# Performance work log

Measured on AMD Instinct MI355X. Metric: run time of the kernel, lower is better.

## Reference

```python
import jax, jax.numpy as jnp
import numpy as np

B, T, D, H = 64, 512, 512, 128

def swish(x):
    return x * jax.nn.sigmoid(x)

def setup_inputs() -> dict:
    key = jax.random.key(0)
    ks = jax.random.split(key, 8)
    X = jax.random.normal(ks[0], (B, T, D), dtype=jnp.float32)
    # strictly-upper-triangular random binary adjacency -> valid DAG
    adj = jax.random.bernoulli(ks[1], 0.3, (T, T)).astype(jnp.float32)
    dag = jnp.triu(adj, k=1)
    s = 1.0 / np.sqrt(D)
    Wk = jax.random.normal(ks[2], (H, D), dtype=jnp.float32) * s
    bk = jax.random.normal(ks[3], (H,), dtype=jnp.float32) * 0.01
    Wq = jax.random.normal(ks[4], (H, D), dtype=jnp.float32) * s
    bq = jax.random.normal(ks[5], (H,), dtype=jnp.float32) * 0.01
    Wv = jax.random.normal(ks[6], (H, D), dtype=jnp.float32) * s
    bv = jax.random.normal(ks[7], (H,), dtype=jnp.float32) * 0.01
    return {"X": X, "dag": dag, "Wk": Wk, "bk": bk, "Wq": Wq, "bq": bq, "Wv": Wv, "bv": bv}

def reference(X, dag, Wk, bk, Wq, bq, Wv, bv):
    K = swish(jnp.einsum('btd,hd->bth', X, Wk) + bk)  # [B,T,H]
    Q = swish(jnp.einsum('btd,hd->bth', X, Wq) + bq)
    V = swish(jnp.einsum('btd,hd->bth', X, Wv) + bv)
    S_qk = jnp.einsum('bqh,bkh->bqk', Q, K) / jnp.sqrt(jnp.float32(H))  # [B,T,T]
    dagT = dag.T  # [T,T]
    Sprime = dagT * jnp.einsum('ij,bjk->bik', dagT, S_qk)  # [B,T,T]
    # masked_fill(Sprime == 0, -inf) then softmax; rows that are all -inf
    # would produce NaN in torch and are replaced by zeros -> do it nan-free.
    nz = Sprime != 0
    masked = jnp.where(nz, Sprime, -jnp.inf)
    row_valid = jnp.any(nz, axis=-1, keepdims=True)  # [B,T,1]
    masked_safe = jnp.where(row_valid, masked, 0.0)
    probs = jax.nn.softmax(masked_safe, axis=-1) * row_valid  # [B,T,T]
    Vprime = jnp.einsum('ij,bjh->bih', dagT, V)  # [B,T,H]
    O = jnp.einsum('bqk,bkh->bqh', probs, V) + Vprime
    return O
```

## Files before the change

kernel.cpp:

```cpp
#include <hip/hip_runtime.h>
#include <hip/hip_bf16.h>

#define Bn 64
#define Tn 512
#define Dn 512
#define Hn 128
#define BT (Bn*Tn)

typedef unsigned short u16;
typedef unsigned long long u64;
typedef __attribute__((ext_vector_type(8))) short bf16x8;
typedef __attribute__((ext_vector_type(4))) float f32x4;

__device__ __forceinline__ u16 f2bf(float f) {
  union { float f; unsigned u; } v; v.f = f;
  unsigned r = (v.u + 0x7FFFu + ((v.u >> 16) & 1u)) >> 16;
  return (u16)r;
}

__device__ __forceinline__ bf16x8 pack8(float4 a, float4 b) {
  bf16x8 o;
  o[0] = (short)f2bf(a.x); o[1] = (short)f2bf(a.y);
  o[2] = (short)f2bf(a.z); o[3] = (short)f2bf(a.w);
  o[4] = (short)f2bf(b.x); o[5] = (short)f2bf(b.y);
  o[6] = (short)f2bf(b.z); o[7] = (short)f2bf(b.w);
  return o;
}

__device__ __forceinline__ void gload16(const void* g, void* lds) {
  __builtin_amdgcn_global_load_lds(
      (const __attribute__((address_space(1))) unsigned int*)g,
      (__attribute__((address_space(3))) unsigned int*)lds, 16, 0, 0);
}

__global__ __launch_bounds__(256) void prep(
    const float4* __restrict__ Wk, const float4* __restrict__ Wq,
    const float4* __restrict__ Wv, ushort4* __restrict__ Wcat,
    const float* __restrict__ dag, u16* __restrict__ dagT,
    u64* __restrict__ bits) {
  __shared__ float s[64][65];
  if (blockIdx.x < 192) {
    int idx = blockIdx.x * 256 + threadIdx.x;
    int which = idx >> 14, j = idx & 16383;
    const float4* src = (which == 0) ? Wk : (which == 1) ? Wq : Wv;
    float4 v = src[j];
    ushort4 o; o.x = f2bf(v.x); o.y = f2bf(v.y); o.z = f2bf(v.z); o.w = f2bf(v.w);
    Wcat[idx] = o;
  } else {
    int bid = blockIdx.x - 192;
    int bx = bid & 7, by = bid >> 3;
    int r0 = by * 64, c0 = bx * 64;
    int t = threadIdx.x;
    int c4 = t & 15, rr = t >> 4;
#pragma unroll
    for (int q = 0; q < 4; ++q) {
      int r = rr + q * 16;
      float4 v = *(const float4*)&dag[(size_t)(r0 + r) * Tn + c0 + c4 * 4];
      s[c4 * 4 + 0][r] = v.x; s[c4 * 4 + 1][r] = v.y;
      s[c4 * 4 + 2][r] = v.z; s[c4 * 4 + 3][r] = v.w;
    }
    __syncthreads();
#pragma unroll
    for (int q = 0; q < 4; ++q) {
      int il = rr + q * 16;
      ushort4 o;
      u64 b4 = 0;
#pragma unroll
      for (int r = 0; r < 4; ++r) {
        float v = s[il][c4 * 4 + r];
        ((u16*)&o)[r] = f2bf(v);
        b4 |= (u64)(v != 0.f) << (c4 * 4 + r);
      }
      *(ushort4*)&dagT[(size_t)(c0 + il) * Tn + r0 + c4 * 4] = o;
      b4 |= __shfl_xor(b4, 1, 64);
      b4 |= __shfl_xor(b4, 2, 64);
      b4 |= __shfl_xor(b4, 4, 64);
      b4 |= __shfl_xor(b4, 8, 64);
      if (c4 == 0) bits[(size_t)(c0 + il) * 8 + (r0 >> 6)] = b4;
    }
  }
}

__global__ __launch_bounds__(256, 2) void qkv3(
    const float* __restrict__ X, const u16* __restrict__ Wcat,
    const float* __restrict__ bk, const float* __restrict__ bq,
    const float* __restrict__ bv,
    u16* __restrict__ Kb, u16* __restrict__ QT, u16* __restrict__ VT) {
  __shared__ u16 sm[28672];
  int bid = blockIdx.x;
  int xcd = bid & 7, idx = bid >> 3;
  int b = (idx & 7) * 8 + xcd;
  int rowblk = idx >> 3;
  int m0 = b * Tn + rowblk * 64;
  int tid = threadIdx.x, lane = tid & 63, wave = tid >> 6;
  int col0 = lane & 15, rg = lane >> 4, kcb = rg * 16;
  int swl = (col0 & 7) << 4;
  int xrow = tid >> 2, xcq = tid & 3;
  f32x4 acc[3][4][2] = {};
  const char* Wb = (const char*)Wcat;
  char* smb = (char*)sm;

#define LOAD_X(kt_)                                                             \
  {                                                                             \
    const float4* s_ = (const float4*)(X + (size_t)(m0 + xrow) * Dn + (kt_) + xcq * 16); \
    xa0 = s_[0]; xa1 = s_[1]; xa2 = s_[2]; xa3 = s_[3];                         \
  }

  float4 xa0, xa1, xa2, xa3;
  LOAD_X(0);
  for (int kt = 0; kt < Dn; kt += 64) {
    {
      int sw = (xrow & 7) << 4;
      *(bf16x8*)(smb + xrow * 128 + ((xcq * 32) ^ sw)) = pack8(xa0, xa1);
      *(bf16x8*)(smb + xrow * 128 + ((xcq * 32 + 16) ^ sw)) = pack8(xa2, xa3);
    }
    if (kt + 64 < Dn) LOAD_X(kt + 64);
#pragma unroll
    for (int q = 0; q < 12; ++q) {
      int c2 = wave * 12 + q;
      int which = c2 >> 4, widx = c2 & 15;
      int flat = widx * 1024 + lane * 16;
      int row = flat >> 7, colb = flat & 127;
      int sw = (row & 7) << 4;
      gload16(Wb + (size_t)which * 131072 + (size_t)row * 1024 + (kt << 1) + (colb ^ sw),
              smb + 8192 + which * 16384 + widx * 1024);
    }
    __syncthreads();
    bf16x8 af[4][2];
#pragma unroll
    for (int m = 0; m < 4; ++m)
#pragma unroll
      for (int kk = 0; kk < 2; ++kk)
        af[m][kk] = *(const bf16x8*)(smb + (m * 16 + col0) * 128 + ((kk * 64 + kcb) ^ swl));
#pragma unroll
    for (int which = 0; which < 3; ++which) {
      bf16x8 bfr[2][2];
#pragma unroll
      for (int n = 0; n < 2; ++n)
#pragma unroll
        for (int kk = 0; kk < 2; ++kk)
          bfr[n][kk] = *(const bf16x8*)(smb + 8192 + which * 16384 +
                                        (wave * 32 + n * 16 + col0) * 128 + ((kk * 64 + kcb) ^ swl));
#pragma unroll
      for (int kk = 0; kk < 2; ++kk)
#pragma unroll
        for (int m = 0; m < 4; ++m)
#pragma unroll
          for (int n = 0; n < 2; ++n)
            acc[which][m][n] = __builtin_amdgcn_mfma_f32_16x16x32_bf16(
                af[m][kk], bfr[n][kk], acc[which][m][n], 0, 0, 0);
    }
    __syncthreads();
  }
#undef LOAD_X

  {
#pragma unroll
    for (int n = 0; n < 2; ++n) {
      int nl = wave * 32 + n * 16 + col0;
      float bsk = bk[nl], bsq = bq[nl], bsv = bv[nl];
#pragma unroll
      for (int m = 0; m < 4; ++m)
#pragma unroll
        for (int r = 0; r < 4; ++r) {
          int tl = m * 16 + rg * 4 + r;
          float xk = acc[0][m][n][r] + bsk;
          float xq = acc[1][m][n][r] + bsq;
          float xv = acc[2][m][n][r] + bsv;
          *(u16*)(smb + tl * 256 + ((nl * 2) ^ ((tl & 7) << 4))) = f2bf(xk / (1.f + __expf(-xk)));
          *(u16*)(smb + 16384 + nl * 128 + ((tl * 2) ^ ((nl & 7) << 4))) = f2bf(xq / (1.f + __expf(-xq)));
          *(u16*)(smb + 32768 + nl * 128 + ((tl * 2) ^ ((nl & 7) << 4))) = f2bf(xv / (1.f + __expf(-xv)));
        }
    }
    __syncthreads();
    int tt0 = rowblk * 64;
#pragma unroll
    for (int p = 0; p < 4; ++p) {
      int c = p * 256 + tid;
      int t = c >> 4, c16 = c & 15;
      *(bf16x8*)&Kb[(size_t)(m0 + t) * Hn + c16 * 8] =
          *(const bf16x8*)(smb + t * 256 + ((c16 * 16) ^ ((t & 7) << 4)));
    }
#pragma unroll
    for (int p = 0; p < 4; ++p) {
      int c = p * 256 + tid;
      int h = c >> 3, c8 = c & 7;
      *(bf16x8*)&QT[((size_t)b * Hn + h) * Tn + tt0 + c8 * 8] =
          *(const bf16x8*)(smb + 16384 + h * 128 + ((c8 * 16) ^ ((h & 7) << 4)));
      *(bf16x8*)&VT[((size_t)b * Hn + h) * Tn + tt0 + c8 * 8] =
          *(const bf16x8*)(smb + 32768 + h * 128 + ((c8 * 16) ^ ((h & 7) << 4)));
    }
  }
}

__global__ __launch_bounds__(256, 2) void dattn(
    const u16* __restrict__ dagT, const u16* __restrict__ QT,
    const u16* __restrict__ VT, const u16* __restrict__ Kb,
    const u64* __restrict__ dbits, float* __restrict__ O) {
  __shared__ char smA[65536];
  __shared__ u16 smQ2[8192];

  int bid = blockIdx.x;
  int xcd = bid & 7, rst = bid >> 3;
  int bx = rst & 7, b = (rst >> 3) * 8 + xcd;
  int m0 = bx * 64;
  int tid = threadIdx.x, lane = tid & 63, wave = tid >> 6;
  int col0 = lane & 15, g = lane >> 4;
  int swl = (col0 & 7) << 4;

  const char* Ab = (const char*)(dagT + (size_t)m0 * Tn);
  const char* Qb = (const char*)(QT + (size_t)b * Hn * Tn);
  const char* Vb = (const char*)(VT + (size_t)b * Hn * Tn);
  const char* Kb0 = (const char*)(Kb + (size_t)b * Tn * Hn);

  f32x4 accq[4][2] = {};
  for (int kt = 0; kt < Tn; kt += 64) {
#pragma unroll
    for (int q = 0; q < 2; ++q) {
      int ch = wave * 2 + q;
      int flat = ch * 1024 + lane * 16;
      int row = flat >> 7, colb = flat & 127;
      int sw = (row & 7) << 4;
      gload16(Ab + (size_t)row * 1024 + kt * 2 + (colb ^ sw), smA + ch * 1024);
    }
#pragma unroll
    for (int q = 0; q < 4; ++q) {
      int ch = wave * 4 + q;
      int flat = ch * 1024 + lane * 16;
      int row = flat >> 7, colb = flat & 127;
      int sw = (row & 7) << 4;
      gload16(Qb + (size_t)row * 1024 + kt * 2 + (colb ^ sw), smA + 8192 + ch * 1024);
    }
    __syncthreads();
    bf16x8 af[4][2], fq[2][2];
#pragma unroll
    for (int m = 0; m < 4; ++m)
#pragma unroll
      for (int kk = 0; kk < 2; ++kk)
        af[m][kk] = *(const bf16x8*)(smA + (m * 16 + col0) * 128 + ((kk * 64 + g * 16) ^ swl));
#pragma unroll
    for (int n = 0; n < 2; ++n)
#pragma unroll
      for (int kk = 0; kk < 2; ++kk)
        fq[n][kk] = *(const bf16x8*)(smA + 8192 + (wave * 32 + n * 16 + col0) * 128 + ((kk * 64 + g * 16) ^ swl));
#pragma unroll
    for (int kk = 0; kk < 2; ++kk)
#pragma unroll
      for (int m = 0; m < 4; ++m)
#pragma unroll
        for (int n = 0; n < 2; ++n)
          accq[m][n] = __builtin_amdgcn_mfma_f32_16x16x32_bf16(af[m][kk], fq[n][kk], accq[m][n], 0, 0, 0);
    __syncthreads();
  }

  const float scale = 0.08838834764831845f;
#pragma unroll
  for (int m = 0; m < 4; ++m)
#pragma unroll
    for (int n = 0; n < 2; ++n)
#pragma unroll
      for (int r = 0; r < 4; ++r) {
        int q = m * 16 + g * 4 + r;
        int h = wave * 32 + n * 16 + col0;
        *(u16*)((char*)smQ2 + q * 256 + ((h * 2) ^ ((q & 7) << 4))) = f2bf(accq[m][n][r] * scale);
      }

#define STAGE_K(c_, buf_)                                                      \
  {                                                                            \
    _Pragma("unroll")                                                          \
    for (int q = 0; q < 8; ++q) {                                              \
      int ch = wave * 8 + q;                                                   \
      int flat = ch * 1024 + lane * 16;                                        \
      int row = flat >> 8, colb = flat & 255;                                  \
      gload16(Kb0 + (size_t)((c_) * 128 + row) * 256 + (colb ^ ((row & 7) << 4)), \
              smA + (buf_) * 32768 + ch * 1024);                               \
    }                                                                          \
  }

  STAGE_K(0, 0);
  __syncthreads();

  int qrow = wave * 16 + col0;
  bf16x8 bq[4];
#pragma unroll
  for (int kk = 0; kk < 4; ++kk)
    bq[kk] = *(const bf16x8*)((char*)smQ2 + qrow * 256 + ((kk * 64 + g * 16) ^ ((qrow & 7) << 4)));
  const u64* dbq = dbits + (size_t)(m0 + qrow) * 8;
  u64 md[8];
#pragma unroll
  for (int w = 0; w < 8; ++w) md[w] = dbq[w];

  f32x4 sa[32] = {};
#pragma unroll
  for (int c = 0; c < 4; ++c) {
    if (c < 3) STAGE_K(c + 1, (c + 1) & 1);
    const char* kb = smA + (c & 1) * 32768;
#pragma unroll
    for (int t = 0; t < 8; ++t)
#pragma unroll
      for (int kk = 0; kk < 4; ++kk) {
        bf16x8 ak = *(const bf16x8*)(kb + (t * 16 + col0) * 256 + ((kk * 64 + g * 16) ^ swl));
        sa[c * 8 + t] = __builtin_amdgcn_mfma_f32_16x16x32_bf16(ak, bq[kk], sa[c * 8 + t], 0, 0, 0);
      }
    if (c < 3) __syncthreads();
  }

  float mx = -INFINITY;
#pragma unroll
  for (int t = 0; t < 32; ++t)
#pragma unroll
    for (int r = 0; r < 4; ++r) {
      int k = t * 16 + g * 4 + r;
      float v = ((md[k >> 6] >> (k & 63)) & 1) ? sa[t][r] : -INFINITY;
      sa[t][r] = v;
      mx = fmaxf(mx, v);
    }
  mx = fmaxf(mx, __shfl_xor(mx, 16, 64));
  mx = fmaxf(mx, __shfl_xor(mx, 32, 64));
  float mm = (mx == -INFINITY) ? 0.f : mx;

  float s = 0.f;
#pragma unroll
  for (int t = 0; t < 32; ++t)
#pragma unroll
    for (int r = 0; r < 4; ++r) {
      float v = sa[t][r];
      float e = (v == -INFINITY) ? 0.f : __expf(v - mm);
      sa[t][r] = e;
      s += e;
    }
  s += __shfl_xor(s, 16, 64);
  s += __shfl_xor(s, 32, 64);
  float inv = (s > 0.f) ? (1.f / s) : 0.f;

  ushort4 pk[32];
#pragma unroll
  for (int t = 0; t < 32; ++t) {
    ushort4 p;
#pragma unroll
    for (int r = 0; r < 4; ++r) {
      int k = t * 16 + g * 4 + r;
      float d = (float)((md[k >> 6] >> (k & 63)) & 1);
      ((u16*)&p)[r] = f2bf(sa[t][r] * inv + d);
    }
    pk[t] = p;
  }

  f32x4 acco[4][2] = {};
  int sww = (qrow & 7) << 4;

#define WRITE_P(c_, base_)                                                     \
  {                                                                            \
    _Pragma("unroll")                                                          \
    for (int tt = 0; tt < 8; ++tt)                                             \
      *(ushort4*)((base_) + qrow * 256 + ((tt * 32 + g * 8) ^ sww)) = pk[(c_) * 8 + tt]; \
  }

  WRITE_P(0, smA);
  __syncthreads();
#pragma unroll
  for (int c = 0; c < 4; ++c) {
    const char* pb = smA + (c & 1) * 16384;
    if (c < 3) WRITE_P(c + 1, smA + ((c + 1) & 1) * 16384);
#pragma unroll
    for (int kk = 0; kk < 4; ++kk) {
      bf16x8 pa[4], vb[2];
#pragma unroll
      for (int m = 0; m < 4; ++m) {
        int row = m * 16 + col0;
        pa[m] = *(const bf16x8*)(pb + row * 256 + ((kk * 64 + g * 16) ^ ((row & 7) << 4)));
      }
#pragma unroll
      for (int n = 0; n < 2; ++n)
        vb[n] = *(const bf16x8*)(Vb + (size_t)(wave * 32 + n * 16 + col0) * 1024 + c * 256 + kk * 64 + g * 16);
#pragma unroll
      for (int m = 0; m < 4; ++m)
#pragma unroll
        for (int n = 0; n < 2; ++n)
          acco[m][n] = __builtin_amdgcn_mfma_f32_16x16x32_bf16(pa[m], vb[n], acco[m][n], 0, 0, 0);
    }
    __syncthreads();
  }

#pragma unroll
  for (int m = 0; m < 4; ++m)
#pragma unroll
    for (int r = 0; r < 4; ++r) {
      int i = m0 + m * 16 + g * 4 + r;
#pragma unroll
      for (int n = 0; n < 2; ++n) {
        int h = wave * 32 + n * 16 + col0;
        O[((size_t)b * Tn + i) * Hn + h] = acco[m][n][r];
      }
    }
#undef STAGE_K
#undef WRITE_P
}

extern "C" void kernel_launch(void* const* d_in, const int* in_sizes, int n_in,
                              void* d_out, int out_size, void* d_ws, size_t ws_size,
                              hipStream_t stream) {
  const float* X   = (const float*)d_in[0];
  const float* dag = (const float*)d_in[1];
  const float* Wk  = (const float*)d_in[2];
  const float* bk  = (const float*)d_in[3];
  const float* Wq  = (const float*)d_in[4];
  const float* bq  = (const float*)d_in[5];
  const float* Wv  = (const float*)d_in[6];
  const float* bv  = (const float*)d_in[7];
  float* O = (float*)d_out;

  char* ws = (char*)d_ws;
  u16* Wcat = (u16*)(ws);
  u16* dagT = (u16*)(ws + 393216);
  u64* dbits= (u64*)(ws + 917504);
  u16* Kb   = (u16*)(ws + 950272);
  u16* QT   = (u16*)(ws + 9338880);
  u16* VT   = (u16*)(ws + 17727488);

  prep<<<256, 256, 0, stream>>>((const float4*)Wk, (const float4*)Wq,
                                (const float4*)Wv, (ushort4*)Wcat, dag, dagT, dbits);
  qkv3<<<BT / 64, 256, 0, stream>>>(X, Wcat, bk, bq, bv, Kb, QT, VT);
  dattn<<<512, 256, 0, stream>>>(dagT, QT, VT, Kb, dbits, O);
}
```

Baseline: 65.83 us.

## Double threads per block in qkv and attention kernels, split key range across wave groups

Both the QKV projection and the attention kernel move from 256 to 512 threads per block, with each wave handling half as many output columns. In the attention kernel, the key dimension is split between two wave groups that each stage half of K and compute half the scores. The softmax row max and row sum are then combined through shared memory with extra barriers. The goal is more waves in flight to hide latency and fewer registers per thread, at the cost of more synchronisation and less fragment reuse per wave.

```diff
diff --git a/kernel.cpp b/kernel.cpp
--- a/kernel.cpp
+++ b/kernel.cpp
@@ -81,7 +81,7 @@
   }
 }
 
-__global__ __launch_bounds__(256, 2) void qkv3(
+__global__ __launch_bounds__(512, 4) void qkv3(
     const float* __restrict__ X, const u16* __restrict__ Wcat,
     const float* __restrict__ bk, const float* __restrict__ bq,
     const float* __restrict__ bv,
@@ -95,29 +95,28 @@
   int tid = threadIdx.x, lane = tid & 63, wave = tid >> 6;
   int col0 = lane & 15, rg = lane >> 4, kcb = rg * 16;
   int swl = (col0 & 7) << 4;
-  int xrow = tid >> 2, xcq = tid & 3;
-  f32x4 acc[3][4][2] = {};
+  int xrow = tid >> 3, xc8 = tid & 7;
+  f32x4 acc[3][4] = {};
   const char* Wb = (const char*)Wcat;
   char* smb = (char*)sm;
 
 #define LOAD_X(kt_)                                                             \
   {                                                                             \
-    const float4* s_ = (const float4*)(X + (size_t)(m0 + xrow) * Dn + (kt_) + xcq * 16); \
-    xa0 = s_[0]; xa1 = s_[1]; xa2 = s_[2]; xa3 = s_[3];                         \
-  }
-
-  float4 xa0, xa1, xa2, xa3;
+    const float4* s_ = (const float4*)(X + (size_t)(m0 + xrow) * Dn + (kt_) + xc8 * 8); \
+    xa0 = s_[0]; xa1 = s_[1];                                                   \
+  }
+
+  float4 xa0, xa1;
   LOAD_X(0);
   for (int kt = 0; kt < Dn; kt += 64) {
     {
       int sw = (xrow & 7) << 4;
-      *(bf16x8*)(smb + xrow * 128 + ((xcq * 32) ^ sw)) = pack8(xa0, xa1);
-      *(bf16x8*)(smb + xrow * 128 + ((xcq * 32 + 16) ^ sw)) = pack8(xa2, xa3);
+      *(bf16x8*)(smb + xrow * 128 + ((xc8 * 16) ^ sw)) = pack8(xa0, xa1);
     }
     if (kt + 64 < Dn) LOAD_X(kt + 64);
 #pragma unroll
-    for (int q = 0; q < 12; ++q) {
-      int c2 = wave * 12 + q;
+    for (int q = 0; q < 6; ++q) {
+      int c2 = wave * 6 + q;
       int which = c2 >> 4, widx = c2 & 15;
       int flat = widx * 1024 + lane * 16;
       int row = flat >> 7, colb = flat & 127;
@@ -134,56 +133,49 @@
         af[m][kk] = *(const bf16x8*)(smb + (m * 16 + col0) * 128 + ((kk * 64 + kcb) ^ swl));
 #pragma unroll
     for (int which = 0; which < 3; ++which) {
-      bf16x8 bfr[2][2];
-#pragma unroll
-      for (int n = 0; n < 2; ++n)
-#pragma unroll
-        for (int kk = 0; kk < 2; ++kk)
-          bfr[n][kk] = *(const bf16x8*)(smb + 8192 + which * 16384 +
-                                        (wave * 32 + n * 16 + col0) * 128 + ((kk * 64 + kcb) ^ swl));
+      bf16x8 bfr[2];
 #pragma unroll
       for (int kk = 0; kk < 2; ++kk)
+        bfr[kk] = *(const bf16x8*)(smb + 8192 + which * 16384 +
+                                   (wave * 16 + col0) * 128 + ((kk * 64 + kcb) ^ swl));
+#pragma unroll
+      for (int kk = 0; kk < 2; ++kk)
 #pragma unroll
         for (int m = 0; m < 4; ++m)
-#pragma unroll
-          for (int n = 0; n < 2; ++n)
-            acc[which][m][n] = __builtin_amdgcn_mfma_f32_16x16x32_bf16(
-                af[m][kk], bfr[n][kk], acc[which][m][n], 0, 0, 0);
+          acc[which][m] = __builtin_amdgcn_mfma_f32_16x16x32_bf16(
+              af[m][kk], bfr[kk], acc[which][m], 0, 0, 0);
     }
     __syncthreads();
   }
 #undef LOAD_X
 
   {
-#pragma unroll
-    for (int n = 0; n < 2; ++n) {
-      int nl = wave * 32 + n * 16 + col0;
-      float bsk = bk[nl], bsq = bq[nl], bsv = bv[nl];
-#pragma unroll
-      for (int m = 0; m < 4; ++m)
-#pragma unroll
-        for (int r = 0; r < 4; ++r) {
-          int tl = m * 16 + rg * 4 + r;
-          float xk = acc[0][m][n][r] + bsk;
-          float xq = acc[1][m][n][r] + bsq;
-          float xv = acc[2][m][n][r] + bsv;
-          *(u16*)(smb + tl * 256 + ((nl * 2) ^ ((tl & 7) << 4))) = f2bf(xk / (1.f + __expf(-xk)));
-          *(u16*)(smb + 16384 + nl * 128 + ((tl * 2) ^ ((nl & 7) << 4))) = f2bf(xq / (1.f + __expf(-xq)));
-          *(u16*)(smb + 32768 + nl * 128 + ((tl * 2) ^ ((nl & 7) << 4))) = f2bf(xv / (1.f + __expf(-xv)));
-        }
-    }
+    int nl = wave * 16 + col0;
+    float bsk = bk[nl], bsq = bq[nl], bsv = bv[nl];
+#pragma unroll
+    for (int m = 0; m < 4; ++m)
+#pragma unroll
+      for (int r = 0; r < 4; ++r) {
+        int tl = m * 16 + rg * 4 + r;
+        float xk = acc[0][m][r] + bsk;
+        float xq = acc[1][m][r] + bsq;
+        float xv = acc[2][m][r] + bsv;
+        *(u16*)(smb + tl * 256 + ((nl * 2) ^ ((tl & 7) << 4))) = f2bf(xk / (1.f + __expf(-xk)));
+        *(u16*)(smb + 16384 + nl * 128 + ((tl * 2) ^ ((nl & 7) << 4))) = f2bf(xq / (1.f + __expf(-xq)));
+        *(u16*)(smb + 32768 + nl * 128 + ((tl * 2) ^ ((nl & 7) << 4))) = f2bf(xv / (1.f + __expf(-xv)));
+      }
     __syncthreads();
     int tt0 = rowblk * 64;
 #pragma unroll
-    for (int p = 0; p < 4; ++p) {
-      int c = p * 256 + tid;
+    for (int p = 0; p < 2; ++p) {
+      int c = p * 512 + tid;
       int t = c >> 4, c16 = c & 15;
       *(bf16x8*)&Kb[(size_t)(m0 + t) * Hn + c16 * 8] =
           *(const bf16x8*)(smb + t * 256 + ((c16 * 16) ^ ((t & 7) << 4)));
     }
 #pragma unroll
-    for (int p = 0; p < 4; ++p) {
-      int c = p * 256 + tid;
+    for (int p = 0; p < 2; ++p) {
+      int c = p * 512 + tid;
       int h = c >> 3, c8 = c & 7;
       *(bf16x8*)&QT[((size_t)b * Hn + h) * Tn + tt0 + c8 * 8] =
           *(const bf16x8*)(smb + 16384 + h * 128 + ((c8 * 16) ^ ((h & 7) << 4)));
@@ -193,7 +185,7 @@
   }
 }
 
-__global__ __launch_bounds__(256, 2) void dattn(
+__global__ __launch_bounds__(512, 4) void dattn(
     const u16* __restrict__ dagT, const u16* __restrict__ QT,
     const u16* __restrict__ VT, const u16* __restrict__ Kb,
     const u64* __restrict__ dbits, float* __restrict__ O) {
@@ -207,49 +199,45 @@
   int tid = threadIdx.x, lane = tid & 63, wave = tid >> 6;
   int col0 = lane & 15, g = lane >> 4;
   int swl = (col0 & 7) << 4;
+  int grp = wave >> 2, gw = wave & 3;
 
   const char* Ab = (const char*)(dagT + (size_t)m0 * Tn);
   const char* Qb = (const char*)(QT + (size_t)b * Hn * Tn);
   const char* Vb = (const char*)(VT + (size_t)b * Hn * Tn);
   const char* Kb0 = (const char*)(Kb + (size_t)b * Tn * Hn);
 
-  f32x4 accq[4][2] = {};
+  f32x4 accq[4] = {};
   for (int kt = 0; kt < Tn; kt += 64) {
+    {
+      int ch = wave;
+      int flat = ch * 1024 + lane * 16;
+      int row = flat >> 7, colb = flat & 127;
+      int sw = (row & 7) << 4;
+      gload16(Ab + (size_t)row * 1024 + kt * 2 + (colb ^ sw), smA + ch * 1024);
+    }
 #pragma unroll
     for (int q = 0; q < 2; ++q) {
       int ch = wave * 2 + q;
       int flat = ch * 1024 + lane * 16;
       int row = flat >> 7, colb = flat & 127;
       int sw = (row & 7) << 4;
-      gload16(Ab + (size_t)row * 1024 + kt * 2 + (colb ^ sw), smA + ch * 1024);
-    }
-#pragma unroll
-    for (int q = 0; q < 4; ++q) {
-      int ch = wave * 4 + q;
-      int flat = ch * 1024 + lane * 16;
-      int row = flat >> 7, colb = flat & 127;
-      int sw = (row & 7) << 4;
       gload16(Qb + (size_t)row * 1024 + kt * 2 + (colb ^ sw), smA + 8192 + ch * 1024);
     }
     __syncthreads();
-    bf16x8 af[4][2], fq[2][2];
+    bf16x8 af[4][2], fq[2];
 #pragma unroll
     for (int m = 0; m < 4; ++m)
 #pragma unroll
       for (int kk = 0; kk < 2; ++kk)
         af[m][kk] = *(const bf16x8*)(smA + (m * 16 + col0) * 128 + ((kk * 64 + g * 16) ^ swl));
 #pragma unroll
-    for (int n = 0; n < 2; ++n)
-#pragma unroll
-      for (int kk = 0; kk < 2; ++kk)
-        fq[n][kk] = *(const bf16x8*)(smA + 8192 + (wave * 32 + n * 16 + col0) * 128 + ((kk * 64 + g * 16) ^ swl));
-#pragma unroll
     for (int kk = 0; kk < 2; ++kk)
+      fq[kk] = *(const bf16x8*)(smA + 8192 + (wave * 16 + col0) * 128 + ((kk * 64 + g * 16) ^ swl));
+#pragma unroll
+    for (int kk = 0; kk < 2; ++kk)
 #pragma unroll
       for (int m = 0; m < 4; ++m)
-#pragma unroll
-        for (int n = 0; n < 2; ++n)
-          accq[m][n] = __builtin_amdgcn_mfma_f32_16x16x32_bf16(af[m][kk], fq[n][kk], accq[m][n], 0, 0, 0);
+        accq[m] = __builtin_amdgcn_mfma_f32_16x16x32_bf16(af[m][kk], fq[kk], accq[m], 0, 0, 0);
     __syncthreads();
   }
 
@@ -257,105 +245,121 @@
 #pragma unroll
   for (int m = 0; m < 4; ++m)
 #pragma unroll
-    for (int n = 0; n < 2; ++n)
-#pragma unroll
-      for (int r = 0; r < 4; ++r) {
-        int q = m * 16 + g * 4 + r;
-        int h = wave * 32 + n * 16 + col0;
-        *(u16*)((char*)smQ2 + q * 256 + ((h * 2) ^ ((q & 7) << 4))) = f2bf(accq[m][n][r] * scale);
-      }
-
-#define STAGE_K(c_, buf_)                                                      \
+    for (int r = 0; r < 4; ++r) {
+      int q = m * 16 + g * 4 + r;
+      int h = wave * 16 + col0;
+      *(u16*)((char*)smQ2 + q * 256 + ((h * 2) ^ ((q & 7) << 4))) = f2bf(accq[m][r] * scale);
+    }
+
+#define STAGE_K(c_)                                                            \
   {                                                                            \
     _Pragma("unroll")                                                          \
-    for (int q = 0; q < 8; ++q) {                                              \
-      int ch = wave * 8 + q;                                                   \
+    for (int q = 0; q < 4; ++q) {                                              \
+      int ch = gw * 4 + q;                                                     \
       int flat = ch * 1024 + lane * 16;                                        \
       int row = flat >> 8, colb = flat & 255;                                  \
-      gload16(Kb0 + (size_t)((c_) * 128 + row) * 256 + (colb ^ ((row & 7) << 4)), \
-              smA + (buf_) * 32768 + ch * 1024);                               \
+      gload16(Kb0 + (size_t)(grp * 256 + (c_) * 64 + row) * 256 + (colb ^ ((row & 7) << 4)), \
+              smA + grp * 32768 + ((c_) & 1) * 16384 + ch * 1024);             \
     }                                                                          \
   }
 
-  STAGE_K(0, 0);
-  __syncthreads();
-
-  int qrow = wave * 16 + col0;
+  STAGE_K(0);
+  __syncthreads();
+
+  int qrow = gw * 16 + col0;
   bf16x8 bq[4];
 #pragma unroll
   for (int kk = 0; kk < 4; ++kk)
     bq[kk] = *(const bf16x8*)((char*)smQ2 + qrow * 256 + ((kk * 64 + g * 16) ^ ((qrow & 7) << 4)));
   const u64* dbq = dbits + (size_t)(m0 + qrow) * 8;
-  u64 md[8];
-#pragma unroll
-  for (int w = 0; w < 8; ++w) md[w] = dbq[w];
-
-  f32x4 sa[32] = {};
+  u64 md[4];
+#pragma unroll
+  for (int w = 0; w < 4; ++w) md[w] = dbq[grp * 4 + w];
+
+  f32x4 sa[16] = {};
 #pragma unroll
   for (int c = 0; c < 4; ++c) {
-    if (c < 3) STAGE_K(c + 1, (c + 1) & 1);
-    const char* kb = smA + (c & 1) * 32768;
-#pragma unroll
-    for (int t = 0; t < 8; ++t)
+    if (c < 3) STAGE_K(c + 1);
+    const char* kb = smA + grp * 32768 + (c & 1) * 16384;
+#pragma unroll
+    for (int t = 0; t < 4; ++t)
 #pragma unroll
       for (int kk = 0; kk < 4; ++kk) {
         bf16x8 ak = *(const bf16x8*)(kb + (t * 16 + col0) * 256 + ((kk * 64 + g * 16) ^ swl));
-        sa[c * 8 + t] = __builtin_amdgcn_mfma_f32_16x16x32_bf16(ak, bq[kk], sa[c * 8 + t], 0, 0, 0);
+        sa[c * 4 + t] = __builtin_amdgcn_mfma_f32_16x16x32_bf16(ak, bq[kk], sa[c * 4 + t], 0, 0, 0);
       }
     if (c < 3) __syncthreads();
   }
 
   float mx = -INFINITY;
 #pragma unroll
-  for (int t = 0; t < 32; ++t)
-#pragma unroll
-    for (int r = 0; r < 4; ++r) {
-      int k = t * 16 + g * 4 + r;
-      float v = ((md[k >> 6] >> (k & 63)) & 1) ? sa[t][r] : -INFINITY;
-      sa[t][r] = v;
-      mx = fmaxf(mx, v);
-    }
+  for (int c = 0; c < 4; ++c)
+#pragma unroll
+    for (int t = 0; t < 4; ++t)
+#pragma unroll
+      for (int r = 0; r < 4; ++r) {
+        int bit = t * 16 + g * 4 + r;
+        float v = ((md[c] >> bit) & 1) ? sa[c * 4 + t][r] : -INFINITY;
+        sa[c * 4 + t][r] = v;
+        mx = fmaxf(mx, v);
+      }
   mx = fmaxf(mx, __shfl_xor(mx, 16, 64));
   mx = fmaxf(mx, __shfl_xor(mx, 32, 64));
-  float mm = (mx == -INFINITY) ? 0.f : mx;
+
+  float* redf = (float*)smQ2;
+  __syncthreads();
+  if (g == 0) redf[qrow * 2 + grp] = mx;
+  __syncthreads();
+  float mboth = fmaxf(redf[qrow * 2], redf[qrow * 2 + 1]);
+  float mm = (mboth == -INFINITY) ? 0.f : mboth;
 
   float s = 0.f;
 #pragma unroll
-  for (int t = 0; t < 32; ++t)
+  for (int i = 0; i < 16; ++i)
 #pragma unroll
     for (int r = 0; r < 4; ++r) {
-      float v = sa[t][r];
+      float v = sa[i][r];
       float e = (v == -INFINITY) ? 0.f : __expf(v - mm);
-      sa[t][r] = e;
+      sa[i][r] = e;
       s += e;
     }
   s += __shfl_xor(s, 16, 64);
   s += __shfl_xor(s, 32, 64);
-  float inv = (s > 0.f) ? (1.f / s) : 0.f;
-
-  ushort4 pk[32];
-#pragma unroll
-  for (int t = 0; t < 32; ++t) {
-    ushort4 p;
-#pragma unroll
-    for (int r = 0; r < 4; ++r) {
-      int k = t * 16 + g * 4 + r;
-      float d = (float)((md[k >> 6] >> (k & 63)) & 1);
-      ((u16*)&p)[r] = f2bf(sa[t][r] * inv + d);
-    }
-    pk[t] = p;
-  }
-
-  f32x4 acco[4][2] = {};
+  if (g == 0) redf[128 + qrow * 2 + grp] = s;
+  __syncthreads();
+  float stot = redf[128 + qrow * 2] + redf[128 + qrow * 2 + 1];
+  float inv = (stot > 0.f) ? (1.f / stot) : 0.f;
+
+  ushort4 pk[16];
+#pragma unroll
+  for (int c = 0; c < 4; ++c)
+#pragma unroll
+    for (int t = 0; t < 4; ++t) {
+      ushort4 p;
+#pragma unroll
+      for (int r = 0; r < 4; ++r) {
+        int bit = t * 16 + g * 4 + r;
+        float d = (float)((md[c] >> bit) & 1);
+        ((u16*)&p)[r] = f2bf(sa[c * 4 + t][r] * inv + d);
+      }
+      pk[c * 4 + t] = p;
+    }
+
+  f32x4 acco[4] = {};
   int sww = (qrow & 7) << 4;
 
 #define WRITE_P(c_, base_)                                                     \
-  {                                                                            \
+  if (grp == ((c_) >> 1)) {                                                    \
+    int cc = (c_) & 1;                                                         \
     _Pragma("unroll")                                                          \
-    for (int tt = 0; tt < 8; ++tt)                                             \
-      *(ushort4*)((base_) + qrow * 256 + ((tt * 32 + g * 8) ^ sww)) = pk[(c_) * 8 + tt]; \
-  }
-
+    for (int u = 0; u < 2; ++u)                                                \
+      _Pragma("unroll")                                                        \
+      for (int t2 = 0; t2 < 4; ++t2)                                           \
+        *(ushort4*)((base_) + qrow * 256 + ((u * 128 + t2 * 32 + g * 8) ^ sww)) = \
+            pk[(cc * 2 + u) * 4 + t2];                                         \
+  }
+
+  __syncthreads();
   WRITE_P(0, smA);
   __syncthreads();
 #pragma unroll
@@ -364,20 +368,16 @@
     if (c < 3) WRITE_P(c + 1, smA + ((c + 1) & 1) * 16384);
 #pragma unroll
     for (int kk = 0; kk < 4; ++kk) {
-      bf16x8 pa[4], vb[2];
+      bf16x8 pa[4], vb;
 #pragma unroll
       for (int m = 0; m < 4; ++m) {
         int row = m * 16 + col0;
         pa[m] = *(const bf16x8*)(pb + row * 256 + ((kk * 64 + g * 16) ^ ((row & 7) << 4)));
       }
-#pragma unroll
-      for (int n = 0; n < 2; ++n)
-        vb[n] = *(const bf16x8*)(Vb + (size_t)(wave * 32 + n * 16 + col0) * 1024 + c * 256 + kk * 64 + g * 16);
+      vb = *(const bf16x8*)(Vb + (size_t)(wave * 16 + col0) * 1024 + c * 256 + kk * 64 + g * 16);
 #pragma unroll
       for (int m = 0; m < 4; ++m)
-#pragma unroll
-        for (int n = 0; n < 2; ++n)
-          acco[m][n] = __builtin_amdgcn_mfma_f32_16x16x32_bf16(pa[m], vb[n], acco[m][n], 0, 0, 0);
+        acco[m] = __builtin_amdgcn_mfma_f32_16x16x32_bf16(pa[m], vb, acco[m], 0, 0, 0);
     }
     __syncthreads();
   }
@@ -387,11 +387,8 @@
 #pragma unroll
     for (int r = 0; r < 4; ++r) {
       int i = m0 + m * 16 + g * 4 + r;
-#pragma unroll
-      for (int n = 0; n < 2; ++n) {
-        int h = wave * 32 + n * 16 + col0;
-        O[((size_t)b * Tn + i) * Hn + h] = acco[m][n][r];
-      }
+      int h = wave * 16 + col0;
+      O[((size_t)b * Tn + i) * Hn + h] = acco[m][r];
     }
 #undef STAGE_K
 #undef WRITE_P
@@ -420,6 +417,6 @@
 
   prep<<<256, 256, 0, stream>>>((const float4*)Wk, (const float4*)Wq,
                                 (const float4*)Wv, (ushort4*)Wcat, dag, dagT, dbits);
-  qkv3<<<BT / 64, 256, 0, stream>>>(X, Wcat, bk, bq, bv, Kb, QT, VT);
-  dattn<<<512, 256, 0, stream>>>(dagT, QT, VT, Kb, dbits, O);
-}
+  qkv3<<<BT / 64, 512, 0, stream>>>(X, Wcat, bk, bq, bv, Kb, QT, VT);
+  dattn<<<512, 512, 0, stream>>>(dagT, QT, VT, Kb, dbits, O);
+}
```

Result: faster. 64.43 us, median of 3 (-2.1%).
